# Kernel tuning notes

Hardware: AMD Instinct MI355X
Metric: run time of the kernel (lower is better)

The kernel has to match this reference:

```python
import jax, jax.numpy as jnp
import numpy as np

E_PHI = 1024
E_F = 1024
HID = 1024
N_HEADS = 16
HEAD_DIM = HID // N_HEADS


def setup_inputs() -> dict:
    key = jax.random.key(0)
    ks = jax.random.split(key, 9)
    B, S = 2, 2048
    s = 0.02
    return {
        "q": jax.random.normal(ks[0], (B, S, E_PHI), jnp.float32),
        "k": jax.random.normal(ks[1], (B, S, E_PHI), jnp.float32),
        "v": jax.random.normal(ks[2], (B, S, E_F), jnp.float32),
        "W_q": jax.random.normal(ks[3], (E_PHI, HID), jnp.float32) * s,
        "W_k": jax.random.normal(ks[4], (E_PHI, HID), jnp.float32) * s,
        "W_v": jax.random.normal(ks[5], (E_F, HID), jnp.float32) * s,
        "b_v": jax.random.normal(ks[6], (HID,), jnp.float32) * s,
        "W_o": jax.random.normal(ks[7], (HID, E_F), jnp.float32) * s,
        "b_o": jax.random.normal(ks[8], (E_F,), jnp.float32) * s,
    }


def reference(q, k, v, W_q, W_k, W_v, b_v, W_o, b_o):
    B, S, _ = q.shape
    # projections -> [B, S, n_heads, head_dim]
    qh = (q @ W_q).reshape(B, S, N_HEADS, HEAD_DIM)
    kh = (k @ W_k).reshape(B, S, N_HEADS, HEAD_DIM)
    vh = (v @ W_v + b_v).reshape(B, S, N_HEADS, HEAD_DIM)

    scale = 1.0 / jnp.sqrt(jnp.float32(HEAD_DIM))
    # scores: [B, H, S_q, S_k]
    scores = jnp.einsum("bihd,bjhd->bhij", qh, kh) * scale

    i = jnp.arange(S)[:, None]
    j = jnp.arange(S)[None, :]
    # strict causal (j < i) plus the single (0,0) entry
    keep = (j < i) | ((i == 0) & (j == 0))
    scores = jnp.where(keep, scores, jnp.float32(-jnp.inf))

    probs = jax.nn.softmax(scores, axis=-1)
    attn = jnp.einsum("bhij,bjhd->bihd", probs, vh).reshape(B, S, HID)
    # dropout is identity in eval mode
    return attn @ W_o + b_o
```

## Files before the change

### kernel.cpp

```cpp
#include <hip/hip_runtime.h>
#include <hip/hip_bf16.h>

typedef __attribute__((ext_vector_type(8))) short bf16x8;
typedef __attribute__((ext_vector_type(4))) float f32x4;
typedef __attribute__((ext_vector_type(4))) unsigned u32x4;

typedef __attribute__((address_space(1))) const void gv_t;
typedef __attribute__((address_space(3))) void lv_t;

static __device__ __forceinline__ void gload16(const void* g, void* l) {
    __builtin_amdgcn_global_load_lds((gv_t*)g, (lv_t*)l, 16, 0, 0);
}

static __device__ __forceinline__ f32x4 mfma16(bf16x8 a, bf16x8 b, f32x4 c) {
    return __builtin_amdgcn_mfma_f32_16x16x32_bf16(a, b, c, 0, 0, 0);
}

static __device__ __forceinline__ unsigned short f2bf(float x) {
    __bf16 b = (__bf16)x;
    return __builtin_bit_cast(unsigned short, b);
}
static __device__ __forceinline__ unsigned pk2(float lo, float hi) {
    return (unsigned)f2bf(lo) | ((unsigned)f2bf(hi) << 16);
}

#define NN 1024
#define KK 1024
#define BK 32
#define NKT (KK / BK)
#define AP 72
#define SOFF2 17.3123404907f

__global__ void cvt3_k(const float* __restrict__ q, const float* __restrict__ k,
                       const float* __restrict__ v, unsigned short* __restrict__ dst)
{
    const int z = blockIdx.y;
    const float* src = (z == 0) ? q : (z == 1) ? k : v;
    unsigned short* d = dst + (size_t)z * 4194304u;
    const size_t i = ((size_t)blockIdx.x * 256 + threadIdx.x) * 8;
    float4 a = *reinterpret_cast<const float4*>(&src[i]);
    float4 b = *reinterpret_cast<const float4*>(&src[i + 4]);
    bf16x8 o;
    o[0] = (short)f2bf(a.x); o[1] = (short)f2bf(a.y);
    o[2] = (short)f2bf(a.z); o[3] = (short)f2bf(a.w);
    o[4] = (short)f2bf(b.x); o[5] = (short)f2bf(b.y);
    o[6] = (short)f2bf(b.z); o[7] = (short)f2bf(b.w);
    *reinterpret_cast<bf16x8*>(&d[i]) = o;
}

__global__ void trcvt_k(const float* __restrict__ w0, const float* __restrict__ w1,
                        const float* __restrict__ w2, const float* __restrict__ w3,
                        unsigned short* __restrict__ dst)
{
    const int z = blockIdx.z;
    const float* W = (z == 0) ? w0 : (z == 1) ? w1 : (z == 2) ? w2 : w3;
    unsigned short* D = dst + (size_t)z * 1048576u;
    __shared__ float t[32][33];
    const int tx = threadIdx.x, ty = threadIdx.y;
    const int x  = blockIdx.x * 32 + tx;
    const int y0 = blockIdx.y * 32;
    for (int i = ty; i < 32; i += 8) t[i][tx] = W[(size_t)(y0 + i) * 1024 + x];
    __syncthreads();
    const int xo = y0 + tx;
    for (int i = ty; i < 32; i += 8)
        D[(size_t)(blockIdx.x * 32 + i) * 1024 + xo] = f2bf(t[tx][i]);
}

__global__ void vtr_k(const unsigned short* __restrict__ vh, unsigned short* __restrict__ vt)
{
    __shared__ unsigned short t[32][33];
    const int bh = blockIdx.z;
    const int b = bh >> 4, h = bh & 15;
    const int s0 = blockIdx.x * 32;
    const int d0 = blockIdx.y * 32;
    const int tx = threadIdx.x, ty = threadIdx.y;
    for (int i = ty; i < 32; i += 8)
        t[i][tx] = vh[(size_t)(b * 2048 + s0 + i) * 1024 + h * 64 + d0 + tx];
    __syncthreads();
    for (int i = ty; i < 32; i += 8)
        vt[((size_t)bh * 64 + d0 + i) * 2048 + s0 + tx] = t[tx][i];
}

template<int MODE>
__global__ __launch_bounds__(256, 2)
void gemm2_k(const unsigned short* __restrict__ Abase,
             const unsigned short* __restrict__ Btbase,
             void* __restrict__ Cbase,
             const float* __restrict__ bias)
{
    __shared__ unsigned short As[3][4096];
    __shared__ unsigned short Bs[3][4096];

    const int f   = blockIdx.x;
    const int xcd = f & 7;
    const int g   = f >> 3;
    const int z   = g >> 5;
    const int rr  = g & 31;
    const int bx  = xcd * 4 + (rr & 3);
    const int by  = rr >> 2;

    const unsigned short* A  = Abase  + (size_t)z * 4194304u;
    const unsigned short* Bt = Btbase + (size_t)z * 1048576u;

    const int tid = threadIdx.x;
    const int wid = tid >> 6, lane = tid & 63;
    const int lg = lane >> 4, lc = lane & 15;
    const int brow = bx * 128;
    const int bcol = by * 128;
    const int wr = (wid >> 1) * 64;
    const int wc = (wid & 1) * 64;

    const int srow = tid >> 2;
    const int scol = (tid & 3) * 8;

    f32x4 acc[4][4];
#pragma unroll
    for (int i = 0; i < 4; ++i)
#pragma unroll
        for (int j = 0; j < 4; ++j) acc[i][j] = (f32x4){0.f, 0.f, 0.f, 0.f};

    auto issue_tile = [&](int kt, int c) {
        const int k0 = kt * BK;
        gload16(&A [(size_t)(brow + srow)      * KK + k0 + scol], &As[c][tid * 8]);
        gload16(&A [(size_t)(brow + 64 + srow) * KK + k0 + scol], &As[c][2048 + tid * 8]);
        gload16(&Bt[(size_t)(bcol + srow)      * KK + k0 + scol], &Bs[c][tid * 8]);
        gload16(&Bt[(size_t)(bcol + 64 + srow) * KK + k0 + scol], &Bs[c][2048 + tid * 8]);
    };
    auto compute_tile = [&](int c) {
        bf16x8 af[4], bfr[4];
#pragma unroll
        for (int i = 0; i < 4; ++i)
            af[i] = *reinterpret_cast<const bf16x8*>(&As[c][(wr + i * 16 + lc) * 32 + lg * 8]);
#pragma unroll
        for (int j = 0; j < 4; ++j)
            bfr[j] = *reinterpret_cast<const bf16x8*>(&Bs[c][(wc + j * 16 + lc) * 32 + lg * 8]);
#pragma unroll
        for (int i = 0; i < 4; ++i)
#pragma unroll
            for (int j = 0; j < 4; ++j)
                acc[i][j] = mfma16(af[i], bfr[j], acc[i][j]);
    };

    issue_tile(0, 0);
    issue_tile(1, 1);

    int c0 = 0, c1 = 1, c2 = 2;
    for (int kt = 0; kt < NKT - 1; ++kt) {
        asm volatile("s_waitcnt vmcnt(4)" ::: "memory");
        __builtin_amdgcn_s_barrier();
        __builtin_amdgcn_sched_barrier(0);
        if (kt + 2 < NKT) issue_tile(kt + 2, c2);
        compute_tile(c0);
        const int t = c0; c0 = c1; c1 = c2; c2 = t;
    }
    asm volatile("s_waitcnt vmcnt(0)" ::: "memory");
    __builtin_amdgcn_s_barrier();
    __builtin_amdgcn_sched_barrier(0);
    compute_tile(c0);

    float scale = 1.0f;
    const float* bp = nullptr;
    if (MODE == 0) { if (z == 0) scale = 0.18033688f; if (z == 2) bp = bias; }
    else           { bp = bias; }

#pragma unroll
    for (int j = 0; j < 4; ++j) {
        const int col = bcol + wc + j * 16 + lc;
        const float bb = bp ? bp[col] : 0.0f;
#pragma unroll
        for (int i = 0; i < 4; ++i) {
            const int row0 = brow + wr + i * 16 + lg * 4;
#pragma unroll
            for (int r = 0; r < 4; ++r) {
                const float val = acc[i][j][r] * scale + bb;
                if (MODE == 0)
                    ((unsigned short*)Cbase)[(size_t)z * 4194304u + (size_t)(row0 + r) * NN + col] = f2bf(val);
                else
                    ((float*)Cbase)[(size_t)(row0 + r) * NN + col] = val;
            }
        }
    }
}

__global__ __launch_bounds__(256, 4)
void attn_k(const unsigned short* __restrict__ qh,
            const unsigned short* __restrict__ kh,
            const unsigned short* __restrict__ vt,
            unsigned short* __restrict__ out)
{
    __shared__ unsigned short Ks[2][64 * AP];
    __shared__ unsigned short Vs[2][64 * AP];

    const int id = blockIdx.x;
    const int u  = id >> 5;
    const int qt = (u < 16) ? u : 47 - u;
    const int bh = (id & 7) * 4 + ((id >> 3) & 3);
    const int b = bh >> 4, h = bh & 15;
    const int tid = threadIdx.x, wid = tid >> 6, lane = tid & 63;
    const int lg = lane >> 4, lc = lane & 15;
    const int q0w = qt * 64 + wid * 16;
    const int hi = lg >> 1;
    const int srcA = ((lg & 1) << 5) | lc;
    const int srcB = srcA + 16;

    const size_t base = (size_t)b * 2048u * 1024u + (size_t)h * 64u;
    const unsigned short* Qb  = qh + base;
    const unsigned short* Kb  = kh + base;
    const unsigned short* Vtb = vt + (size_t)bh * 131072u;

    const int r0 = tid >> 3, kof = (tid & 7) * 8;

    bf16x8 qf[2];
#pragma unroll
    for (int s = 0; s < 2; ++s)
        qf[s] = *reinterpret_cast<const bf16x8*>(&Qb[(size_t)(q0w + lc) * 1024 + s * 32 + lg * 8]);

    f32x4 accT[4];
#pragma unroll
    for (int d = 0; d < 4; ++d) accT[d] = (f32x4){0.f, 0.f, 0.f, 0.f};
    float lsum = 0.f;

    bf16x8 ka0 = *reinterpret_cast<const bf16x8*>(&Kb [(size_t)(r0)      * 1024 + kof]);
    bf16x8 ka1 = *reinterpret_cast<const bf16x8*>(&Kb [(size_t)(32 + r0) * 1024 + kof]);
    bf16x8 va0 = *reinterpret_cast<const bf16x8*>(&Vtb[(size_t)(r0)      * 2048 + kof]);
    bf16x8 va1 = *reinterpret_cast<const bf16x8*>(&Vtb[(size_t)(32 + r0) * 2048 + kof]);

    for (int kt = 0; kt <= qt; ++kt) {
        const int cur = kt & 1;
        const int k0 = kt * 64;

        *reinterpret_cast<bf16x8*>(&Ks[cur][(r0)      * AP + kof]) = ka0;
        *reinterpret_cast<bf16x8*>(&Ks[cur][(32 + r0) * AP + kof]) = ka1;
        *reinterpret_cast<bf16x8*>(&Vs[cur][(r0)      * AP + kof]) = va0;
        *reinterpret_cast<bf16x8*>(&Vs[cur][(32 + r0) * AP + kof]) = va1;
        asm volatile("s_waitcnt lgkmcnt(0)" ::: "memory");
        __builtin_amdgcn_s_barrier();
        __builtin_amdgcn_sched_barrier(0);

        if (kt < qt) {
            const int kn = k0 + 64;
            ka0 = *reinterpret_cast<const bf16x8*>(&Kb [(size_t)(kn + r0)      * 1024 + kof]);
            ka1 = *reinterpret_cast<const bf16x8*>(&Kb [(size_t)(kn + 32 + r0) * 1024 + kof]);
            va0 = *reinterpret_cast<const bf16x8*>(&Vtb[(size_t)(r0)      * 2048 + kn + kof]);
            va1 = *reinterpret_cast<const bf16x8*>(&Vtb[(size_t)(32 + r0) * 2048 + kn + kof]);
        }

        f32x4 sc[4];
#pragma unroll
        for (int g = 0; g < 4; ++g) sc[g] = (f32x4){0.f, 0.f, 0.f, 0.f};
        __builtin_amdgcn_s_setprio(1);
#pragma unroll
        for (int s = 0; s < 2; ++s)
#pragma unroll
            for (int g = 0; g < 4; ++g) {
                bf16x8 kf = *reinterpret_cast<const bf16x8*>(
                    &Ks[cur][(g * 16 + lc) * AP + s * 32 + lg * 8]);
                sc[g] = mfma16(kf, qf[s], sc[g]);
            }
        __builtin_amdgcn_s_setprio(0);

        if (kt == qt) {
            const int qi = q0w + lc;
#pragma unroll
            for (int g = 0; g < 4; ++g)
#pragma unroll
                for (int r = 0; r < 4; ++r) {
                    const int ki = k0 + g * 16 + lg * 4 + r;
                    const bool keep = (ki < qi) || (qi == 0 && ki == 0);
                    if (!keep) sc[g][r] = -1e30f;
                }
        }

        float p[4][4];
#pragma unroll
        for (int g = 0; g < 4; ++g)
#pragma unroll
            for (int r = 0; r < 4; ++r) {
                p[g][r] = exp2f(sc[g][r] - SOFF2);
                lsum += p[g][r];
            }

        unsigned w[4][2];
#pragma unroll
        for (int g = 0; g < 4; ++g) {
            w[g][0] = pk2(p[g][0], p[g][1]);
            w[g][1] = pk2(p[g][2], p[g][3]);
        }

#pragma unroll
        for (int s = 0; s < 2; ++s) {
            unsigned a0A = __shfl(w[2 * s][0],     srcA);
            unsigned a1A = __shfl(w[2 * s][1],     srcA);
            unsigned b0A = __shfl(w[2 * s][0],     srcB);
            unsigned b1A = __shfl(w[2 * s][1],     srcB);
            unsigned a0B = __shfl(w[2 * s + 1][0], srcA);
            unsigned a1B = __shfl(w[2 * s + 1][1], srcA);
            unsigned b0B = __shfl(w[2 * s + 1][0], srcB);
            unsigned b1B = __shfl(w[2 * s + 1][1], srcB);
            u32x4 fr;
            fr[0] = hi ? a0B : a0A;
            fr[1] = hi ? a1B : a1A;
            fr[2] = hi ? b0B : b0A;
            fr[3] = hi ? b1B : b1A;
            bf16x8 pb = __builtin_bit_cast(bf16x8, fr);
            __builtin_amdgcn_s_setprio(1);
#pragma unroll
            for (int di = 0; di < 4; ++di) {
                bf16x8 vf = *reinterpret_cast<const bf16x8*>(
                    &Vs[cur][(di * 16 + lc) * AP + s * 32 + lg * 8]);
                accT[di] = mfma16(vf, pb, accT[di]);
            }
            __builtin_amdgcn_s_setprio(0);
        }
    }

    lsum += __shfl_xor(lsum, 16);
    lsum += __shfl_xor(lsum, 32);
    const float inv = 1.0f / lsum;

    const size_t orow = (size_t)(b * 2048 + q0w + lc) * 1024 + (size_t)h * 64 + lg * 4;
#pragma unroll
    for (int di = 0; di < 4; ++di) {
        unsigned lo  = pk2(accT[di][0] * inv, accT[di][1] * inv);
        unsigned hi2 = pk2(accT[di][2] * inv, accT[di][3] * inv);
        uint2 st; st.x = lo; st.y = hi2;
        *reinterpret_cast<uint2*>(&out[orow + di * 16]) = st;
    }
}

extern "C" void kernel_launch(void* const* d_in, const int* in_sizes, int n_in,
                              void* d_out, int out_size, void* d_ws, size_t ws_size,
                              hipStream_t stream)
{
    const float* q   = (const float*)d_in[0];
    const float* k   = (const float*)d_in[1];
    const float* v   = (const float*)d_in[2];
    const float* W_q = (const float*)d_in[3];
    const float* W_k = (const float*)d_in[4];
    const float* W_v = (const float*)d_in[5];
    const float* b_v = (const float*)d_in[6];
    const float* W_o = (const float*)d_in[7];
    const float* b_o = (const float*)d_in[8];

    char* w = (char*)d_ws;
    unsigned short* qkvb = (unsigned short*)w;
    unsigned short* Wt   = (unsigned short*)(w + 25165824);
    unsigned short* ph   = (unsigned short*)(w + 33554432);
    unsigned short* attn = (unsigned short*)(w + 58720256);
    unsigned short* vt   = qkvb;

    cvt3_k <<<dim3(2048, 3, 1), 256, 0, stream>>>(q, k, v, qkvb);
    trcvt_k<<<dim3(32, 32, 4), dim3(32, 8, 1), 0, stream>>>(W_q, W_k, W_v, W_o, Wt);
    gemm2_k<0><<<dim3(768, 1, 1), 256, 0, stream>>>(qkvb, Wt, ph, b_v);
    vtr_k  <<<dim3(64, 2, 32), dim3(32, 8, 1), 0, stream>>>(ph + 2 * 4194304, vt);
    attn_k <<<dim3(1024, 1, 1), 256, 0, stream>>>(ph, ph + 4194304, vt, attn);
    gemm2_k<1><<<dim3(256, 1, 1), 256, 0, stream>>>(attn, Wt + 3 * 1048576, d_out, b_o);
}
```

Before: 126.5 us.

## Load K/V fragments directly from global in attention and retile output GEMM

The attention kernel drops its LDS double-buffering of K and V tiles and its per-iteration barriers, reading MFMA fragments straight from global memory (relying on L1/L2 reuse across the four waves). The output-projection GEMM gains a 64-row tile variant with a 512-block grid and adjusted XCD mapping to fill more CUs, and the QKV GEMM's launch bounds rise to 3 blocks per SM. The attention change removes barrier and LDS-store overhead but issues four times the global/cache traffic per block and loses coalesced loads.

```diff
diff --git a/kernel.cpp b/kernel.cpp
--- a/kernel.cpp
+++ b/kernel.cpp
@@ -28,7 +28,6 @@
 #define KK 1024
 #define BK 32
 #define NKT (KK / BK)
-#define AP 72
 #define SOFF2 17.3123404907f
 
 __global__ void cvt3_k(const float* __restrict__ q, const float* __restrict__ k,
@@ -81,23 +80,32 @@
         vt[((size_t)bh * 64 + d0 + i) * 2048 + s0 + tx] = t[tx][i];
 }
 
-template<int MODE>
-__global__ __launch_bounds__(256, 2)
+template<int MODE, int TM, int MINB>
+__global__ __launch_bounds__(256, MINB)
 void gemm2_k(const unsigned short* __restrict__ Abase,
              const unsigned short* __restrict__ Btbase,
              void* __restrict__ Cbase,
              const float* __restrict__ bias)
 {
-    __shared__ unsigned short As[3][4096];
+    constexpr int ACH = TM / 64;
+    constexpr int NJ  = (TM == 128) ? 4 : 2;
+    __shared__ unsigned short As[3][ACH * 2048];
     __shared__ unsigned short Bs[3][4096];
 
     const int f   = blockIdx.x;
     const int xcd = f & 7;
     const int g   = f >> 3;
-    const int z   = g >> 5;
-    const int rr  = g & 31;
-    const int bx  = xcd * 4 + (rr & 3);
-    const int by  = rr >> 2;
+    int z, bx, by;
+    if (MODE == 0) {
+        z  = g >> 5;
+        const int rr = g & 31;
+        bx = xcd * 4 + (rr & 3);
+        by = rr >> 2;
+    } else {
+        z  = 0;
+        bx = xcd * 8 + (g & 7);
+        by = g >> 3;
+    }
 
     const unsigned short* A  = Abase  + (size_t)z * 4194304u;
     const unsigned short* Bt = Btbase + (size_t)z * 1048576u;
@@ -105,39 +113,40 @@
     const int tid = threadIdx.x;
     const int wid = tid >> 6, lane = tid & 63;
     const int lg = lane >> 4, lc = lane & 15;
-    const int brow = bx * 128;
+    const int brow = bx * TM;
     const int bcol = by * 128;
-    const int wr = (wid >> 1) * 64;
-    const int wc = (wid & 1) * 64;
+    const int wr = (TM == 128) ? (wid >> 1) * 64 : 0;
+    const int wc = (TM == 128) ? (wid & 1) * 64  : wid * 32;
 
     const int srow = tid >> 2;
     const int scol = (tid & 3) * 8;
 
-    f32x4 acc[4][4];
+    f32x4 acc[4][NJ];
 #pragma unroll
     for (int i = 0; i < 4; ++i)
 #pragma unroll
-        for (int j = 0; j < 4; ++j) acc[i][j] = (f32x4){0.f, 0.f, 0.f, 0.f};
+        for (int j = 0; j < NJ; ++j) acc[i][j] = (f32x4){0.f, 0.f, 0.f, 0.f};
 
     auto issue_tile = [&](int kt, int c) {
         const int k0 = kt * BK;
-        gload16(&A [(size_t)(brow + srow)      * KK + k0 + scol], &As[c][tid * 8]);
-        gload16(&A [(size_t)(brow + 64 + srow) * KK + k0 + scol], &As[c][2048 + tid * 8]);
+#pragma unroll
+        for (int ch = 0; ch < ACH; ++ch)
+            gload16(&A[(size_t)(brow + ch * 64 + srow) * KK + k0 + scol], &As[c][ch * 2048 + tid * 8]);
         gload16(&Bt[(size_t)(bcol + srow)      * KK + k0 + scol], &Bs[c][tid * 8]);
         gload16(&Bt[(size_t)(bcol + 64 + srow) * KK + k0 + scol], &Bs[c][2048 + tid * 8]);
     };
     auto compute_tile = [&](int c) {
-        bf16x8 af[4], bfr[4];
+        bf16x8 af[4], bfr[NJ];
 #pragma unroll
         for (int i = 0; i < 4; ++i)
             af[i] = *reinterpret_cast<const bf16x8*>(&As[c][(wr + i * 16 + lc) * 32 + lg * 8]);
 #pragma unroll
-        for (int j = 0; j < 4; ++j)
+        for (int j = 0; j < NJ; ++j)
             bfr[j] = *reinterpret_cast<const bf16x8*>(&Bs[c][(wc + j * 16 + lc) * 32 + lg * 8]);
 #pragma unroll
         for (int i = 0; i < 4; ++i)
 #pragma unroll
-            for (int j = 0; j < 4; ++j)
+            for (int j = 0; j < NJ; ++j)
                 acc[i][j] = mfma16(af[i], bfr[j], acc[i][j]);
     };
 
@@ -146,7 +155,8 @@
 
     int c0 = 0, c1 = 1, c2 = 2;
     for (int kt = 0; kt < NKT - 1; ++kt) {
-        asm volatile("s_waitcnt vmcnt(4)" ::: "memory");
+        if (TM == 128) asm volatile("s_waitcnt vmcnt(4)" ::: "memory");
+        else           asm volatile("s_waitcnt vmcnt(3)" ::: "memory");
         __builtin_amdgcn_s_barrier();
         __builtin_amdgcn_sched_barrier(0);
         if (kt + 2 < NKT) issue_tile(kt + 2, c2);
@@ -164,7 +174,7 @@
     else           { bp = bias; }
 
 #pragma unroll
-    for (int j = 0; j < 4; ++j) {
+    for (int j = 0; j < NJ; ++j) {
         const int col = bcol + wc + j * 16 + lc;
         const float bb = bp ? bp[col] : 0.0f;
 #pragma unroll
@@ -188,9 +198,6 @@
             const unsigned short* __restrict__ vt,
             unsigned short* __restrict__ out)
 {
-    __shared__ unsigned short Ks[2][64 * AP];
-    __shared__ unsigned short Vs[2][64 * AP];
-
     const int id = blockIdx.x;
     const int u  = id >> 5;
     const int qt = (u < 16) ? u : 47 - u;
@@ -208,42 +215,21 @@
     const unsigned short* Kb  = kh + base;
     const unsigned short* Vtb = vt + (size_t)bh * 131072u;
 
-    const int r0 = tid >> 3, kof = (tid & 7) * 8;
-
     bf16x8 qf[2];
 #pragma unroll
     for (int s = 0; s < 2; ++s)
         qf[s] = *reinterpret_cast<const bf16x8*>(&Qb[(size_t)(q0w + lc) * 1024 + s * 32 + lg * 8]);
 
+    const unsigned short* Krow = Kb + (size_t)lc * 1024 + lg * 8;
+    const unsigned short* Vrow = Vtb + (size_t)lc * 2048 + lg * 8;
+
     f32x4 accT[4];
 #pragma unroll
     for (int d = 0; d < 4; ++d) accT[d] = (f32x4){0.f, 0.f, 0.f, 0.f};
     float lsum = 0.f;
 
-    bf16x8 ka0 = *reinterpret_cast<const bf16x8*>(&Kb [(size_t)(r0)      * 1024 + kof]);
-    bf16x8 ka1 = *reinterpret_cast<const bf16x8*>(&Kb [(size_t)(32 + r0) * 1024 + kof]);
-    bf16x8 va0 = *reinterpret_cast<const bf16x8*>(&Vtb[(size_t)(r0)      * 2048 + kof]);
-    bf16x8 va1 = *reinterpret_cast<const bf16x8*>(&Vtb[(size_t)(32 + r0) * 2048 + kof]);
-
     for (int kt = 0; kt <= qt; ++kt) {
-        const int cur = kt & 1;
         const int k0 = kt * 64;
-
-        *reinterpret_cast<bf16x8*>(&Ks[cur][(r0)      * AP + kof]) = ka0;
-        *reinterpret_cast<bf16x8*>(&Ks[cur][(32 + r0) * AP + kof]) = ka1;
-        *reinterpret_cast<bf16x8*>(&Vs[cur][(r0)      * AP + kof]) = va0;
-        *reinterpret_cast<bf16x8*>(&Vs[cur][(32 + r0) * AP + kof]) = va1;
-        asm volatile("s_waitcnt lgkmcnt(0)" ::: "memory");
-        __builtin_amdgcn_s_barrier();
-        __builtin_amdgcn_sched_barrier(0);
-
-        if (kt < qt) {
-            const int kn = k0 + 64;
-            ka0 = *reinterpret_cast<const bf16x8*>(&Kb [(size_t)(kn + r0)      * 1024 + kof]);
-            ka1 = *reinterpret_cast<const bf16x8*>(&Kb [(size_t)(kn + 32 + r0) * 1024 + kof]);
-            va0 = *reinterpret_cast<const bf16x8*>(&Vtb[(size_t)(r0)      * 2048 + kn + kof]);
-            va1 = *reinterpret_cast<const bf16x8*>(&Vtb[(size_t)(32 + r0) * 2048 + kn + kof]);
-        }
 
         f32x4 sc[4];
 #pragma unroll
@@ -254,7 +240,7 @@
 #pragma unroll
             for (int g = 0; g < 4; ++g) {
                 bf16x8 kf = *reinterpret_cast<const bf16x8*>(
-                    &Ks[cur][(g * 16 + lc) * AP + s * 32 + lg * 8]);
+                    &Krow[(size_t)(k0 + g * 16) * 1024 + s * 32]);
                 sc[g] = mfma16(kf, qf[s], sc[g]);
             }
         __builtin_amdgcn_s_setprio(0);
@@ -307,7 +293,7 @@
 #pragma unroll
             for (int di = 0; di < 4; ++di) {
                 bf16x8 vf = *reinterpret_cast<const bf16x8*>(
-                    &Vs[cur][(di * 16 + lc) * AP + s * 32 + lg * 8]);
+                    &Vrow[(size_t)(di * 16) * 2048 + k0 + s * 32]);
                 accT[di] = mfma16(vf, pb, accT[di]);
             }
             __builtin_amdgcn_s_setprio(0);
@@ -351,8 +337,8 @@
 
     cvt3_k <<<dim3(2048, 3, 1), 256, 0, stream>>>(q, k, v, qkvb);
     trcvt_k<<<dim3(32, 32, 4), dim3(32, 8, 1), 0, stream>>>(W_q, W_k, W_v, W_o, Wt);
-    gemm2_k<0><<<dim3(768, 1, 1), 256, 0, stream>>>(qkvb, Wt, ph, b_v);
+    gemm2_k<0, 128, 3><<<dim3(768, 1, 1), 256, 0, stream>>>(qkvb, Wt, ph, b_v);
     vtr_k  <<<dim3(64, 2, 32), dim3(32, 8, 1), 0, stream>>>(ph + 2 * 4194304, vt);
     attn_k <<<dim3(1024, 1, 1), 256, 0, stream>>>(ph, ph + 4194304, vt, attn);
-    gemm2_k<1><<<dim3(256, 1, 1), 256, 0, stream>>>(attn, Wt + 3 * 1048576, d_out, b_o);
-}
+    gemm2_k<1, 64, 2><<<dim3(512, 1, 1), 256, 0, stream>>>(attn, Wt + 3 * 1048576, d_out, b_o);
+}
```

New measurement: 210.2 us. 1.66x slower.
